# Kernel optimization log

Measured on AMD Instinct MI355X. Metric: run time of the kernel, lower is better.

## Reference

```python
import jax, jax.numpy as jnp
import numpy as np

B, N, D, OUT = 32, 4096, 512, 512
LN_EPS = 1e-5
EPS = 1e-8


def _layernorm(x, g, b):
    m = jnp.mean(x, axis=-1, keepdims=True)
    v = jnp.mean((x - m) ** 2, axis=-1, keepdims=True)
    return (x - m) * jax.lax.rsqrt(v + LN_EPS) * g + b


def setup_inputs() -> dict:
    key = jax.random.key(0)
    ks = jax.random.split(key, 12)
    x = jax.random.normal(ks[0], (B, N, D), dtype=jnp.float32)
    mask = jax.random.bernoulli(ks[1], 0.9, (B, N))
    mask = mask.at[:, 0].set(True)  # guarantee no fully-masked row
    h = D // 4
    s = lambda fan_in: 1.0 / np.sqrt(fan_in)
    return {
        "x": x,
        "mask": mask,
        # attention MLP: Linear(D, D//4) -> tanh -> Linear(D//4, 1)
        "attn_w1": jax.random.normal(ks[2], (D, h), jnp.float32) * s(D),
        "attn_b1": jnp.zeros((h,), jnp.float32),
        "attn_w2": jax.random.normal(ks[3], (h, 1), jnp.float32) * s(h),
        "attn_b2": jnp.zeros((1,), jnp.float32),
        # gate: Linear(3D, D) -> LN -> GELU -> Linear(D, 3) -> softmax
        "gate_w1": jax.random.normal(ks[4], (3 * D, D), jnp.float32) * s(3 * D),
        "gate_b1": jnp.zeros((D,), jnp.float32),
        "gate_ln_g": jnp.ones((D,), jnp.float32),
        "gate_ln_b": jnp.zeros((D,), jnp.float32),
        "gate_w2": jax.random.normal(ks[5], (D, 3), jnp.float32) * s(D),
        "gate_b2": jnp.zeros((3,), jnp.float32),
        # out_proj: Linear(D, OUT) -> LN -> Dropout(eval: identity)
        "out_w": jax.random.normal(ks[6], (D, OUT), jnp.float32) * s(D),
        "out_b": jnp.zeros((OUT,), jnp.float32),
        "out_ln_g": jnp.ones((OUT,), jnp.float32),
        "out_ln_b": jnp.zeros((OUT,), jnp.float32),
    }


def reference(x, mask, attn_w1, attn_b1, attn_w2, attn_b2,
              gate_w1, gate_b1, gate_ln_g, gate_ln_b, gate_w2, gate_b2,
              out_w, out_b, out_ln_g, out_ln_b):
    # attention scores: [B, N]
    h = jnp.tanh(jnp.einsum('bnd,dh->bnh', x, attn_w1) + attn_b1)
    scores = (jnp.einsum('bnh,ho->bno', h, attn_w2) + attn_b2)[..., 0]
    scores = jnp.where(mask, scores, -jnp.inf)
    attn_w = jax.nn.softmax(scores, axis=-1)
    attn_w = jnp.nan_to_num(attn_w, nan=0.0)
    attn_pooled = jnp.einsum('bnd,bn->bd', x, attn_w)

    # masked max pool
    x_masked = jnp.where(mask[..., None], x, -jnp.inf)
    max_pooled = jnp.max(x_masked, axis=1)
    max_pooled = jnp.nan_to_num(max_pooled, nan=0.0, posinf=0.0, neginf=0.0)

    # masked mean pool
    mfl = mask.astype(x.dtype)
    masked_sum = jnp.einsum('bnd,bn->bd', x, mfl)
    num_valid = jnp.clip(jnp.sum(mfl, axis=1, keepdims=True), EPS, None)
    mean_pooled = masked_sum / num_valid

    # gated combine
    combined = jnp.concatenate([attn_pooled, max_pooled, mean_pooled], axis=-1)
    g = combined @ gate_w1 + gate_b1
    g = _layernorm(g, gate_ln_g, gate_ln_b)
    g = jax.nn.gelu(g, approximate=False)
    gates = jax.nn.softmax(g @ gate_w2 + gate_b2, axis=-1)  # [B, 3]

    stacked = jnp.stack([attn_pooled, max_pooled, mean_pooled], axis=2)  # [B, D, 3]
    weighted = jnp.einsum('bdk,bk->bd', stacked, gates)

    out = weighted @ out_w + out_b
    out = _layernorm(out, out_ln_g, out_ln_b)  # dropout: eval mode -> identity
    return out
```

## Files before the change

### kernel.cpp

```cpp
#include <hip/hip_runtime.h>
#include <hip/hip_bf16.h>
#include <math.h>

#define BB 32
#define NN 4096
#define DD 512
#define HH 128
#define NCH 128
#define LN_EPS 1e-5f
#define MEPS 1e-8f

typedef __attribute__((ext_vector_type(8))) short bf16x8;
typedef __attribute__((ext_vector_type(4))) float f32x4;

__device__ __forceinline__ unsigned pk_bf16(float a, float b) {
    unsigned ua = __float_as_uint(a); ua = (ua + 0x7FFFu + ((ua >> 16) & 1u)) >> 16;
    unsigned ub = __float_as_uint(b); ub = (ub + 0x7FFFu + ((ub >> 16) & 1u)) >> 16;
    return ua | (ub << 16);
}
__device__ __forceinline__ unsigned short bf16_1(float a) {
    unsigned ua = __float_as_uint(a);
    return (unsigned short)((ua + 0x7FFFu + ((ua >> 16) & 1u)) >> 16);
}
__device__ __forceinline__ float bflo(unsigned u) { return __uint_as_float(u << 16); }
__device__ __forceinline__ float bfhi(unsigned u) { return __uint_as_float(u & 0xFFFF0000u); }

__global__ __launch_bounds__(256) void gmsp_prep(
    const void* __restrict__ mask, unsigned char* __restrict__ m8,
    const float* __restrict__ w1, unsigned short* __restrict__ w1f)
{
    int blk = blockIdx.x, t = threadIdx.x;
    if (blk < 512) {
        __shared__ int sf[2];
        const unsigned* mu = (const unsigned*)mask;
        bool f32f = false, i8f = false;
#pragma unroll
        for (int i = 0; i < 4; ++i) {
            unsigned v = mu[t + i * 256];
            f32f |= (v == 0x3F800000u);
            i8f  |= (v > 1u) && (v != 0x3F800000u);
        }
        if (t == 0) { sf[0] = 0; sf[1] = 0; }
        __syncthreads();
        int wf32 = __any((int)f32f), wi8 = __any((int)i8f);
        if ((t & 63) == 0) {
            if (wf32) atomicOr(&sf[0], 1);
            if (wi8)  atomicOr(&sf[1], 1);
        }
        __syncthreads();
        int fmt = sf[0] ? 2 : (sf[1] ? 1 : 0);
        int i = blk * 256 + t;
        unsigned char v;
        if (fmt == 1)      v = ((const unsigned char*)mask)[i] != 0;
        else if (fmt == 2) v = ((const float*)mask)[i] != 0.0f;
        else               v = ((const int*)mask)[i] != 0;
        m8[i] = v;
    } else {
        int idx = (blk - 512) * 256 + t;
        int j = idx & 7;
        int e = idx >> 3;
        int lane = e & 63;
        int half = (e >> 6) & 1;
        int s = (e >> 7) & 15;
        int g2 = (e >> 11) & 3;
        int h = g2 * 32 + half * 16 + (lane & 15);
        int k = s * 32 + (lane >> 4) * 8 + j;
        w1f[(size_t)e * 8 + j] = bf16_1(w1[(size_t)k * HH + h]);
    }
}

__global__ __launch_bounds__(256, 4) void gmsp_fused(
    const float* __restrict__ x, const unsigned short* __restrict__ w1f,
    const float* __restrict__ b1, const float* __restrict__ w2,
    const float* __restrict__ b2, const unsigned char* __restrict__ m8,
    float* __restrict__ attnp, float* __restrict__ sump, float* __restrict__ maxp,
    float* __restrict__ mc, float* __restrict__ sc, float* __restrict__ cnt)
{
    __shared__ char At[32 * 1024];
    __shared__ float sred[32][4] __attribute__((aligned(16)));
    __shared__ float wrow[32];
    __shared__ float cpool[2][512];

    const int t = threadIdx.x;
    const int lane = t & 63, wid = t >> 6;
    const int l15 = lane & 15, lq = (lane >> 4) & 3;
    const int blk = blockIdx.x;
    const int b = blk >> 7, ch = blk & 127;
    const size_t row0 = (size_t)b * NN + (size_t)ch * 32;

    float4 sreg[16];
    {
        const float4* xb = (const float4*)(x + row0 * DD);
#pragma unroll
        for (int j = 0; j < 16; ++j) sreg[j] = xb[j * 256 + t];
    }
    uint4 mq0 = *(const uint4*)(m8 + row0);
    uint4 mq1 = *(const uint4*)(m8 + row0 + 16);
    unsigned mwa[8] = {mq0.x, mq0.y, mq0.z, mq0.w, mq1.x, mq1.y, mq1.z, mq1.w};

    const int H = t >> 7;
    const int c4 = t & 127;
    float ps[4] = {0.f, 0.f, 0.f, 0.f};
    float pm[4] = {-INFINITY, -INFINITY, -INFINITY, -INFINITY};
#pragma unroll
    for (int j = 0; j < 16; ++j) {
        const int row = 2 * j + H;
        float4 v = sreg[j];
        uint2 pw; pw.x = pk_bf16(v.x, v.y); pw.y = pk_bf16(v.z, v.w);
        *(uint2*)(At + row * 1024 + ((c4 * 8) ^ ((row & 7) << 4))) = pw;
        int mv = (mwa[j >> 1] >> ((2 * (j & 1) + H) * 8)) & 0xFF;
        if (mv) {
            ps[0] += v.x; ps[1] += v.y; ps[2] += v.z; ps[3] += v.w;
            pm[0] = fmaxf(pm[0], v.x); pm[1] = fmaxf(pm[1], v.y);
            pm[2] = fmaxf(pm[2], v.z); pm[3] = fmaxf(pm[3], v.w);
        }
    }
    __syncthreads();

    const int hb = wid * 32;
    f32x4 acc00 = (f32x4)0.f, acc01 = (f32x4)0.f, acc10 = (f32x4)0.f, acc11 = (f32x4)0.f;
    {
        const char* wf = (const char*)w1f + (size_t)wid * 32768 + (size_t)lane * 16;
        const char* ar0 = At + l15 * 1024;
        const char* ar1 = At + (16 + l15) * 1024;
        const int swz = (l15 & 7) << 4;
#pragma unroll
        for (int s = 0; s < 16; ++s) {
            bf16x8 bf0 = *(const bf16x8*)(wf + s * 2048);
            bf16x8 bf1 = *(const bf16x8*)(wf + s * 2048 + 1024);
            const int co = (s * 64 + lq * 16) ^ swz;
            bf16x8 a0 = *(const bf16x8*)(ar0 + co);
            bf16x8 a1 = *(const bf16x8*)(ar1 + co);
            acc00 = __builtin_amdgcn_mfma_f32_16x16x32_bf16(a0, bf0, acc00, 0, 0, 0);
            acc01 = __builtin_amdgcn_mfma_f32_16x16x32_bf16(a0, bf1, acc01, 0, 0, 0);
            acc10 = __builtin_amdgcn_mfma_f32_16x16x32_bf16(a1, bf0, acc10, 0, 0, 0);
            acc11 = __builtin_amdgcn_mfma_f32_16x16x32_bf16(a1, bf1, acc11, 0, 0, 0);
        }
    }
    {
        const float b10 = b1[hb + l15], b11 = b1[hb + 16 + l15];
        const float w20 = w2[hb + l15], w21 = w2[hb + 16 + l15];
#pragma unroll
        for (int rf = 0; rf < 2; ++rf) {
            f32x4 aA = rf ? acc10 : acc00;
            f32x4 aB = rf ? acc11 : acc01;
#pragma unroll
            for (int r = 0; r < 4; ++r) {
                float p0 = fminf(fmaxf(aA[r] + b10, -10.f), 10.f);
                float p1 = fminf(fmaxf(aB[r] + b11, -10.f), 10.f);
                float e0 = __expf(2.f * p0), e1 = __expf(2.f * p1);
                float v = (e0 - 1.f) / (e0 + 1.f) * w20 + (e1 - 1.f) / (e1 + 1.f) * w21;
                v += __shfl_xor(v, 1); v += __shfl_xor(v, 2);
                v += __shfl_xor(v, 4); v += __shfl_xor(v, 8);
                if (l15 == 0) sred[rf * 16 + lq * 4 + r][wid] = v;
            }
        }
    }
    __syncthreads();

    if (t < 32) {
        float4 s4 = *(const float4*)&sred[t][0];
        float ssum = s4.x + s4.y + s4.z + s4.w + b2[0];
        int valid = m8[row0 + t];
        float score = valid ? ssum : -INFINITY;
        float mx = score;
        mx = fmaxf(mx, __shfl_xor(mx, 1));  mx = fmaxf(mx, __shfl_xor(mx, 2));
        mx = fmaxf(mx, __shfl_xor(mx, 4));  mx = fmaxf(mx, __shfl_xor(mx, 8));
        mx = fmaxf(mx, __shfl_xor(mx, 16));
        float e = valid ? __expf(score - mx) : 0.f;
        wrow[t] = e;
        float ts = e, tc = valid ? 1.f : 0.f;
        ts += __shfl_xor(ts, 1);  tc += __shfl_xor(tc, 1);
        ts += __shfl_xor(ts, 2);  tc += __shfl_xor(tc, 2);
        ts += __shfl_xor(ts, 4);  tc += __shfl_xor(tc, 4);
        ts += __shfl_xor(ts, 8);  tc += __shfl_xor(tc, 8);
        ts += __shfl_xor(ts, 16); tc += __shfl_xor(tc, 16);
        if (t == 0) { mc[blk] = mx; sc[blk] = ts; cnt[blk] = tc; }
    }
    __syncthreads();

    float a0 = 0.f, a1 = 0.f;
#pragma unroll 8
    for (int r = 0; r < 32; ++r) {
        float w = wrow[r];
        unsigned u = *(const unsigned*)(At + r * 1024 + ((t * 4) ^ ((r & 7) << 4)));
        a0 = fmaf(w, bflo(u), a0);
        a1 = fmaf(w, bfhi(u), a1);
    }

    *(float4*)&cpool[H][c4 * 4] = make_float4(ps[0], ps[1], ps[2], ps[3]);
    __syncthreads();
    float sv0 = cpool[0][2 * t] + cpool[1][2 * t];
    float sv1 = cpool[0][2 * t + 1] + cpool[1][2 * t + 1];
    __syncthreads();
    *(float4*)&cpool[H][c4 * 4] = make_float4(pm[0], pm[1], pm[2], pm[3]);
    __syncthreads();
    float mv0 = fmaxf(cpool[0][2 * t], cpool[1][2 * t]);
    float mv1 = fmaxf(cpool[0][2 * t + 1], cpool[1][2 * t + 1]);

    const size_t ob = (size_t)blk * DD + 2 * t;
    *(float2*)(attnp + ob) = make_float2(a0, a1);
    *(float2*)(sump + ob)  = make_float2(sv0, sv1);
    *(float2*)(maxp + ob)  = make_float2(mv0, mv1);
}

__device__ __forceinline__ float gmsp_block_sum(float v, float* red, int t) {
    __syncthreads();
    red[t] = v; __syncthreads();
    for (int s = 128; s > 0; s >>= 1) { if (t < s) red[t] += red[t + s]; __syncthreads(); }
    return red[0];
}
__device__ __forceinline__ float gmsp_block_max(float v, float* red, int t) {
    __syncthreads();
    red[t] = v; __syncthreads();
    for (int s = 128; s > 0; s >>= 1) { if (t < s) red[t] = fmaxf(red[t], red[t + s]); __syncthreads(); }
    return red[0];
}

__global__ __launch_bounds__(256) void gmsp_tail(
    const float* __restrict__ attnp, const float* __restrict__ sump,
    const float* __restrict__ maxp, const float* __restrict__ mc,
    const float* __restrict__ sc, const float* __restrict__ cnt,
    const float* __restrict__ gate_w1, const float* __restrict__ gate_b1,
    const float* __restrict__ gln_g, const float* __restrict__ gln_b,
    const float* __restrict__ gate_w2, const float* __restrict__ gate_b2,
    const float* __restrict__ out_w, const float* __restrict__ out_b,
    const float* __restrict__ oln_g, const float* __restrict__ oln_b,
    float* __restrict__ out)
{
    __shared__ float comb[3 * DD];
    __shared__ float wvec[DD];
    __shared__ float red[256];
    __shared__ float ef[NCH];
    __shared__ float part[2][DD];
    int b = blockIdx.x, t = threadIdx.x;

    float mcv = (t < NCH) ? mc[b * NCH + t] : -INFINITY;
    float M = gmsp_block_max(mcv, red, t);
    float e = (t < NCH && mcv != -INFINITY) ? __expf(mcv - M) : 0.f;
    if (t < NCH) ef[t] = e;
    float T = gmsp_block_sum(e * ((t < NCH) ? sc[b * NCH + t] : 0.f), red, t);
    float C = gmsp_block_sum((t < NCH) ? cnt[b * NCH + t] : 0.f, red, t);
    float invT = T > 0.f ? 1.f / T : 0.f;
    C = fmaxf(C, MEPS);
    __syncthreads();

    int d0 = 2 * t;
    float ax = 0.f, ay = 0.f, sx = 0.f, sy = 0.f, mx = -INFINITY, my = -INFINITY;
    for (int c = 0; c < NCH; ++c) {
        size_t base = (size_t)(b * NCH + c) * DD + d0;
        float2 av = *(const float2*)(attnp + base);
        float2 sv = *(const float2*)(sump + base);
        float2 xv = *(const float2*)(maxp + base);
        float ec = ef[c];
        ax = fmaf(ec, av.x, ax); ay = fmaf(ec, av.y, ay);
        sx += sv.x; sy += sv.y;
        mx = fmaxf(mx, xv.x); my = fmaxf(my, xv.y);
    }
    ax *= invT; ay *= invT;
    float icnt = 1.f / C;
    float meanx = sx * icnt, meany = sy * icnt;
    if (isinf(mx)) mx = 0.f;
    if (isinf(my)) my = 0.f;

    comb[d0] = ax;               comb[d0 + 1] = ay;
    comb[DD + d0] = mx;          comb[DD + d0 + 1] = my;
    comb[2 * DD + d0] = meanx;   comb[2 * DD + d0 + 1] = meany;
    __syncthreads();

    const int th = t & 127, kh = t >> 7;
    {
        float4 g4 = make_float4(0.f, 0.f, 0.f, 0.f);
        const float* gw = gate_w1 + (size_t)kh * 768 * DD + th * 4;
        for (int k = 0; k < 768; ++k) {
            float cv = comb[kh * 768 + k];
            float4 wv = *(const float4*)(gw + (size_t)k * DD);
            g4.x = fmaf(cv, wv.x, g4.x); g4.y = fmaf(cv, wv.y, g4.y);
            g4.z = fmaf(cv, wv.z, g4.z); g4.w = fmaf(cv, wv.w, g4.w);
        }
        *(float4*)&part[kh][th * 4] = g4;
    }
    __syncthreads();
    float gx = part[0][d0] + part[1][d0] + gate_b1[d0];
    float gy = part[0][d0 + 1] + part[1][d0 + 1] + gate_b1[d0 + 1];

    float mg = gmsp_block_sum(gx + gy, red, t) * (1.f / DD);
    float vg = gmsp_block_sum(gx * gx + gy * gy, red, t) * (1.f / DD) - mg * mg;
    float inv = rsqrtf(vg + LN_EPS);
    gx = (gx - mg) * inv * gln_g[d0] + gln_b[d0];
    gy = (gy - mg) * inv * gln_g[d0 + 1] + gln_b[d0 + 1];
    gx = 0.5f * gx * (1.f + erff(gx * 0.70710678118654752f));
    gy = 0.5f * gy * (1.f + erff(gy * 0.70710678118654752f));

    float p0 = gx * gate_w2[d0 * 3 + 0] + gy * gate_w2[(d0 + 1) * 3 + 0];
    float p1 = gx * gate_w2[d0 * 3 + 1] + gy * gate_w2[(d0 + 1) * 3 + 1];
    float p2 = gx * gate_w2[d0 * 3 + 2] + gy * gate_w2[(d0 + 1) * 3 + 2];
    float l0 = gmsp_block_sum(p0, red, t) + gate_b2[0];
    float l1 = gmsp_block_sum(p1, red, t) + gate_b2[1];
    float l2 = gmsp_block_sum(p2, red, t) + gate_b2[2];
    float mxl = fmaxf(l0, fmaxf(l1, l2));
    float e0 = __expf(l0 - mxl), e1 = __expf(l1 - mxl), e2 = __expf(l2 - mxl);
    float ie = 1.f / (e0 + e1 + e2);
    float gw0 = e0 * ie, gw1 = e1 * ie, gw2 = e2 * ie;

    wvec[d0]     = ax * gw0 + mx * gw1 + meanx * gw2;
    wvec[d0 + 1] = ay * gw0 + my * gw1 + meany * gw2;
    __syncthreads();

    {
        float4 o4 = make_float4(0.f, 0.f, 0.f, 0.f);
        const float* ow = out_w + (size_t)kh * 256 * DD + th * 4;
        for (int k = 0; k < 256; ++k) {
            float wvk = wvec[kh * 256 + k];
            float4 w4 = *(const float4*)(ow + (size_t)k * DD);
            o4.x = fmaf(wvk, w4.x, o4.x); o4.y = fmaf(wvk, w4.y, o4.y);
            o4.z = fmaf(wvk, w4.z, o4.z); o4.w = fmaf(wvk, w4.w, o4.w);
        }
        *(float4*)&part[kh][th * 4] = o4;
    }
    __syncthreads();
    float ox = part[0][d0] + part[1][d0] + out_b[d0];
    float oy = part[0][d0 + 1] + part[1][d0 + 1] + out_b[d0 + 1];

    float mo = gmsp_block_sum(ox + oy, red, t) * (1.f / DD);
    float vo = gmsp_block_sum(ox * ox + oy * oy, red, t) * (1.f / DD) - mo * mo;
    float io = rsqrtf(vo + LN_EPS);
    float2 res;
    res.x = (ox - mo) * io * oln_g[d0] + oln_b[d0];
    res.y = (oy - mo) * io * oln_g[d0 + 1] + oln_b[d0 + 1];
    *(float2*)(out + (size_t)b * DD + d0) = res;
}

extern "C" void kernel_launch(void* const* d_in, const int* in_sizes, int n_in,
                              void* d_out, int out_size, void* d_ws, size_t ws_size,
                              hipStream_t stream) {
    const float* x        = (const float*)d_in[0];
    const void*  mask     = d_in[1];
    const float* attn_w1  = (const float*)d_in[2];
    const float* attn_b1  = (const float*)d_in[3];
    const float* attn_w2  = (const float*)d_in[4];
    const float* attn_b2  = (const float*)d_in[5];
    const float* gate_w1  = (const float*)d_in[6];
    const float* gate_b1  = (const float*)d_in[7];
    const float* gln_g    = (const float*)d_in[8];
    const float* gln_b    = (const float*)d_in[9];
    const float* gate_w2  = (const float*)d_in[10];
    const float* gate_b2  = (const float*)d_in[11];
    const float* out_w    = (const float*)d_in[12];
    const float* out_b    = (const float*)d_in[13];
    const float* oln_g    = (const float*)d_in[14];
    const float* oln_b    = (const float*)d_in[15];
    float* out = (float*)d_out;

    char* p = (char*)d_ws;
    unsigned char* m8 = (unsigned char*)p;      p += (size_t)BB * NN;
    unsigned short* w1f = (unsigned short*)p;   p += (size_t)DD * HH * 2;
    float* attnp = (float*)p;                   p += (size_t)BB * NCH * DD * 4;
    float* sump = (float*)p;                    p += (size_t)BB * NCH * DD * 4;
    float* maxp = (float*)p;                    p += (size_t)BB * NCH * DD * 4;
    float* mc = (float*)p;                      p += (size_t)BB * NCH * 4;
    float* sc = (float*)p;                      p += (size_t)BB * NCH * 4;
    float* cnt = (float*)p;                     p += (size_t)BB * NCH * 4;

    gmsp_prep<<<768, 256, 0, stream>>>(mask, m8, attn_w1, w1f);
    gmsp_fused<<<BB * NCH, 256, 0, stream>>>(x, w1f, attn_b1, attn_w2, attn_b2, m8,
                                             attnp, sump, maxp, mc, sc, cnt);
    gmsp_tail<<<BB, 256, 0, stream>>>(attnp, sump, maxp, mc, sc, cnt,
                                      gate_w1, gate_b1, gln_g, gln_b, gate_w2, gate_b2,
                                      out_w, out_b, oln_g, oln_b, out);
}
```

Measured before the change: 147.7 us.

## Drop LDS staging and barriers in fused pooling, write half-partials to global

Every wave now computes the per-row softmax weights redundantly and broadcasts them with __shfl instead of going through shared memory, which removes one barrier. The in-block combine of the two half-row sum/max partials via shared memory, along with three barriers, is also removed. Both halves are written straight to global memory, so the sum and max partial buffers double in size and the tail kernel now reduces over twice as many chunks. This trades fewer block syncs and less LDS use for extra global writes and reads.

```diff
diff --git a/kernel.cpp b/kernel.cpp
--- a/kernel.cpp
+++ b/kernel.cpp
@@ -78,8 +78,6 @@
 {
     __shared__ char At[32 * 1024];
     __shared__ float sred[32][4] __attribute__((aligned(16)));
-    __shared__ float wrow[32];
-    __shared__ float cpool[2][512];
 
     const int t = threadIdx.x;
     const int lane = t & 63, wid = t >> 6;
@@ -158,18 +156,19 @@
     }
     __syncthreads();
 
-    if (t < 32) {
-        float4 s4 = *(const float4*)&sred[t][0];
-        float ssum = s4.x + s4.y + s4.z + s4.w + b2[0];
-        int valid = m8[row0 + t];
-        float score = valid ? ssum : -INFINITY;
+    float wv;
+    {
+        const int rl = lane & 31;
+        float4 s4 = *(const float4*)&sred[rl][0];
+        float ssc = s4.x + s4.y + s4.z + s4.w + b2[0];
+        bool val = m8[row0 + rl] != 0;
+        float score = val ? ssc : -INFINITY;
         float mx = score;
         mx = fmaxf(mx, __shfl_xor(mx, 1));  mx = fmaxf(mx, __shfl_xor(mx, 2));
         mx = fmaxf(mx, __shfl_xor(mx, 4));  mx = fmaxf(mx, __shfl_xor(mx, 8));
         mx = fmaxf(mx, __shfl_xor(mx, 16));
-        float e = valid ? __expf(score - mx) : 0.f;
-        wrow[t] = e;
-        float ts = e, tc = valid ? 1.f : 0.f;
+        wv = val ? __expf(score - mx) : 0.f;
+        float ts = wv, tc = val ? 1.f : 0.f;
         ts += __shfl_xor(ts, 1);  tc += __shfl_xor(tc, 1);
         ts += __shfl_xor(ts, 2);  tc += __shfl_xor(tc, 2);
         ts += __shfl_xor(ts, 4);  tc += __shfl_xor(tc, 4);
@@ -177,31 +176,20 @@
         ts += __shfl_xor(ts, 16); tc += __shfl_xor(tc, 16);
         if (t == 0) { mc[blk] = mx; sc[blk] = ts; cnt[blk] = tc; }
     }
-    __syncthreads();
 
     float a0 = 0.f, a1 = 0.f;
 #pragma unroll 8
     for (int r = 0; r < 32; ++r) {
-        float w = wrow[r];
+        float w = __shfl(wv, r);
         unsigned u = *(const unsigned*)(At + r * 1024 + ((t * 4) ^ ((r & 7) << 4)));
         a0 = fmaf(w, bflo(u), a0);
         a1 = fmaf(w, bfhi(u), a1);
     }
-
-    *(float4*)&cpool[H][c4 * 4] = make_float4(ps[0], ps[1], ps[2], ps[3]);
-    __syncthreads();
-    float sv0 = cpool[0][2 * t] + cpool[1][2 * t];
-    float sv1 = cpool[0][2 * t + 1] + cpool[1][2 * t + 1];
-    __syncthreads();
-    *(float4*)&cpool[H][c4 * 4] = make_float4(pm[0], pm[1], pm[2], pm[3]);
-    __syncthreads();
-    float mv0 = fmaxf(cpool[0][2 * t], cpool[1][2 * t]);
-    float mv1 = fmaxf(cpool[0][2 * t + 1], cpool[1][2 * t + 1]);
-
-    const size_t ob = (size_t)blk * DD + 2 * t;
-    *(float2*)(attnp + ob) = make_float2(a0, a1);
-    *(float2*)(sump + ob)  = make_float2(sv0, sv1);
-    *(float2*)(maxp + ob)  = make_float2(mv0, mv1);
+    *(float2*)(attnp + (size_t)blk * DD + 2 * t) = make_float2(a0, a1);
+
+    const size_t pb = ((size_t)blk * 2 + H) * DD + 4 * c4;
+    *(float4*)(sump + pb) = make_float4(ps[0], ps[1], ps[2], ps[3]);
+    *(float4*)(maxp + pb) = make_float4(pm[0], pm[1], pm[2], pm[3]);
 }
 
 __device__ __forceinline__ float gmsp_block_sum(float v, float* red, int t) {
@@ -246,14 +234,17 @@
     __syncthreads();
 
     int d0 = 2 * t;
-    float ax = 0.f, ay = 0.f, sx = 0.f, sy = 0.f, mx = -INFINITY, my = -INFINITY;
+    float ax = 0.f, ay = 0.f;
     for (int c = 0; c < NCH; ++c) {
-        size_t base = (size_t)(b * NCH + c) * DD + d0;
-        float2 av = *(const float2*)(attnp + base);
+        float2 av = *(const float2*)(attnp + (size_t)(b * NCH + c) * DD + d0);
+        float ec = ef[c];
+        ax = fmaf(ec, av.x, ax); ay = fmaf(ec, av.y, ay);
+    }
+    float sx = 0.f, sy = 0.f, mx = -INFINITY, my = -INFINITY;
+    for (int c = 0; c < 2 * NCH; ++c) {
+        size_t base = (size_t)(b * 2 * NCH + c) * DD + d0;
         float2 sv = *(const float2*)(sump + base);
         float2 xv = *(const float2*)(maxp + base);
-        float ec = ef[c];
-        ax = fmaf(ec, av.x, ax); ay = fmaf(ec, av.y, ay);
         sx += sv.x; sy += sv.y;
         mx = fmaxf(mx, xv.x); my = fmaxf(my, xv.y);
     }
@@ -356,8 +347,8 @@
     unsigned char* m8 = (unsigned char*)p;      p += (size_t)BB * NN;
     unsigned short* w1f = (unsigned short*)p;   p += (size_t)DD * HH * 2;
     float* attnp = (float*)p;                   p += (size_t)BB * NCH * DD * 4;
-    float* sump = (float*)p;                    p += (size_t)BB * NCH * DD * 4;
-    float* maxp = (float*)p;                    p += (size_t)BB * NCH * DD * 4;
+    float* sump = (float*)p;                    p += (size_t)BB * NCH * 2 * DD * 4;
+    float* maxp = (float*)p;                    p += (size_t)BB * NCH * 2 * DD * 4;
     float* mc = (float*)p;                      p += (size_t)BB * NCH * 4;
     float* sc = (float*)p;                      p += (size_t)BB * NCH * 4;
     float* cnt = (float*)p;                     p += (size_t)BB * NCH * 4;
```

Measured after the change: 155.8 us. +5.5%, slower.
